# Performance work log

Hardware: AMD Instinct MI355X
Metric: run time of the kernel (lower is better)

## Reference

```python
import jax, jax.numpy as jnp
import numpy as np

# MX microscaling decode helpers. Codes are stored as int32 holding uint8 bit patterns.
_FP4_MAG = jnp.array([0.0, 0.5, 1.0, 1.5, 2.0, 3.0, 4.0, 6.0], dtype=jnp.float32)  # E2M1

def dec_fp4(c):
    # c in [0,16): bit3 = sign, bits0-2 index E2M1 magnitude LUT
    s = jnp.where(c >= 8, -1.0, 1.0)
    return s * _FP4_MAG[c & 7]

def dec_fp6(c):
    # E3M2, bias 3. bit5 sign, bits2-4 exp, bits0-1 mantissa
    s = jnp.where(c >= 32, -1.0, 1.0)
    e = ((c >> 2) & 7).astype(jnp.float32)
    m = (c & 3).astype(jnp.float32)
    mag = jnp.where(e == 0, m * 0.25 * 0.25, (1.0 + m * 0.25) * jnp.exp2(e - 3.0))
    return s * mag

def dec_fp8(c):
    # E4M3, bias 7. bit7 sign, bits3-6 exp, bits0-2 mantissa (NaN code decoded as 480, consistent both sides)
    s = jnp.where(c >= 128, -1.0, 1.0)
    e = ((c >> 3) & 15).astype(jnp.float32)
    m = (c & 7).astype(jnp.float32)
    mag = jnp.where(e == 0, m * 0.125 * jnp.exp2(-6.0), (1.0 + m * 0.125) * jnp.exp2(e - 7.0))
    return s * mag

def unpack4(p):
    # [..., K//2] bytes -> [..., K] nibbles; low nibble = even element, high = odd
    lo = p & 15
    hi = (p >> 4) & 15
    return jnp.stack([lo, hi], axis=-1).reshape(*p.shape[:-1], p.shape[-1] * 2)

def unpack6(p):
    # little-endian 6-bit packing: 4 values per 3 bytes. [..., K*6//8] -> [..., K]
    g = p.reshape(*p.shape[:-1], -1, 3)
    b0, b1, b2 = g[..., 0], g[..., 1], g[..., 2]
    v0 = b0 & 0x3F
    v1 = ((b0 >> 6) & 3) | ((b1 & 0x0F) << 2)
    v2 = ((b1 >> 4) & 0x0F) | ((b2 & 3) << 4)
    v3 = (b2 >> 2) & 0x3F
    return jnp.stack([v0, v1, v2, v3], axis=-1).reshape(*p.shape[:-1], p.shape[-1] * 4 // 3)

def blockscale(x, sf):
    # x [..., K] fp32, sf [..., K//32] E8M0 exponents: scale = 2^(sf-127) per 32-element block
    scale = jnp.exp2(sf.astype(jnp.float32) - 127.0)
    xs = x.reshape(*x.shape[:-1], -1, 32) * scale[..., None]
    return xs.reshape(x.shape)

def dequant(codes, sf, bits):
    if bits == 4:
        x = dec_fp4(unpack4(codes))
    elif bits == 6:
        x = dec_fp6(unpack6(codes))
    else:
        x = dec_fp8(codes)
    return blockscale(x, sf)


def setup_inputs() -> dict:
    key = jax.random.key(0)
    ks = jax.random.split(key, 13)
    M, N = 4096, 4096
    p4, p6, p8 = 3072, 768, 256
    ri = lambda k, sh: jax.random.randint(k, sh, 0, 256, dtype=jnp.int32)
    sf = lambda k, sh: jax.random.randint(k, sh, 121, 132, dtype=jnp.int32)
    return {
        "AN": ri(ks[0], (M, p4 // 2)),
        "AS": ri(ks[1], (M, p6 * 6 // 8)),
        "AO": ri(ks[2], (M, p8)),
        "SFAN": sf(ks[3], (M, p4 // 32)),
        "SFAS": sf(ks[4], (M, p6 // 32)),
        "SFAO": sf(ks[5], (M, p8 // 32)),
        "BN": ri(ks[6], (N, p4 // 2)),
        "BS": ri(ks[7], (N, p6 * 6 // 8)),
        "BO": ri(ks[8], (N, p8)),
        "SFBN": sf(ks[9], (N * p4 // 32,)),
        "SFBS": sf(ks[10], (N * p6 // 32,)),
        "SFBO": sf(ks[11], (N * p8 // 32,)),
        "bias": jax.random.normal(ks[12], (N,), dtype=jnp.float32) * 0.02,
    }


def reference(AN, AS, AO, SFAN, SFAS, SFAO, BN, BS, BO, SFBN, SFBS, SFBO, bias):
    N = BN.shape[0]
    a4 = dequant(AN, SFAN, 4)                       # [M, p4]
    w4 = dequant(BN, SFBN.reshape(N, -1), 4)        # [N, p4]
    a6 = dequant(AS, SFAS, 6)                       # [M, p6]
    w6 = dequant(BS, SFBS.reshape(N, -1), 6)        # [N, p6]
    a8 = dequant(AO, SFAO, 8)                       # [M, p8]
    w8 = dequant(BO, SFBO.reshape(N, -1), 8)        # [N, p8]
    y = a4 @ w4.T + a6 @ w6.T + a8 @ w8.T           # [M, N]
    return y + bias
```

## Files before the change

### kernel.cpp

```cpp
#include <hip/hip_runtime.h>

typedef short short8 __attribute__((ext_vector_type(8)));
typedef int   intx8  __attribute__((ext_vector_type(8)));
typedef float floatx16 __attribute__((ext_vector_type(16)));

__device__ __forceinline__ unsigned pk4(int a, int b, int c, int d) {
    return (a & 255) | ((b & 255) << 8) | ((c & 255) << 16) | ((unsigned)(d & 255) << 24);
}

__device__ __forceinline__ unsigned dec8bf(int c, int esf) {
    int s = (c & 128) << 8;
    int e = (c >> 3) & 15, m = c & 7;
    int rn = s | ((e + 120 + esf) << 7) | (m << 4);
    int nb = (m >= 4) ? 2 : ((m >= 2) ? 1 : 0);
    int rs = m ? (s | ((nb + 118 + esf) << 7) | ((m << (7 - nb)) & 0x7F)) : s;
    return (unsigned)(e ? rn : rs);
}

__device__ __forceinline__ void pack_one(
    int t, const int* __restrict__ Pn, const int* __restrict__ Ps, const int* __restrict__ Po,
    const int* __restrict__ Sn, const int* __restrict__ Ss, const int* __restrict__ So,
    unsigned char* __restrict__ C4, unsigned char* __restrict__ C6,
    unsigned short* __restrict__ C8, unsigned char* __restrict__ St, int R)
{
    int T0 = R * 48, T1 = T0 + R * 24, T2 = T1 + R * 8, T3 = T2 + R * 24, T4 = T3 + R * 12;
    if (t < T0) {
        int jj = t / R, r = t - jj * R;
        const int4* p = (const int4*)(Pn + (size_t)r * 1536 + jj * 32);
        #pragma unroll
        for (int h = 0; h < 2; ++h) {
            uint4 o; unsigned* po = (unsigned*)&o;
            #pragma unroll
            for (int q = 0; q < 4; q++) { int4 b = p[4 * h + q]; po[q] = pk4(b.x, b.y, b.z, b.w); }
            *(uint4*)(C4 + ((size_t)(2 * jj + h) * R + r) * 16) = o;
        }
    } else if (t < T1) {
        t -= T0; int g = t / R, r = t - g * R;
        const int4* p = (const int4*)(Ps + (size_t)r * 576 + g * 24);
        unsigned d[6];
        #pragma unroll
        for (int q = 0; q < 6; q++) { int4 b = p[q]; d[q] = pk4(b.x, b.y, b.z, b.w); }
        unsigned char* dst = C6 + ((size_t)g * R + r) * 24;
        *(int2*)(dst)      = (int2){ (int)d[0], (int)d[1] };
        *(int2*)(dst + 8)  = (int2){ (int)d[2], (int)d[3] };
        *(int2*)(dst + 16) = (int2){ (int)d[4], (int)d[5] };
    } else if (t < T2) {
        t -= T1; int jj = t / R, r = t - jj * R;
        const int4* p = (const int4*)(Po + (size_t)r * 256 + jj * 32);
        int e = So[r * 8 + jj] - 127;
        #pragma unroll
        for (int cq = 0; cq < 4; ++cq) {
            int4 c0 = p[2 * cq], c1 = p[2 * cq + 1];
            int cs[8] = { c0.x, c0.y, c0.z, c0.w, c1.x, c1.y, c1.z, c1.w };
            uint4 o; unsigned* po = (unsigned*)&o;
            #pragma unroll
            for (int i = 0; i < 4; i++)
                po[i] = dec8bf(cs[2 * i] & 255, e) | (dec8bf(cs[2 * i + 1] & 255, e) << 16);
            *(uint4*)((unsigned char*)C8 + ((size_t)(4 * jj + cq) * R + r) * 16) = o;
        }
    } else if (t < T3) {
        t -= T2; int q = t / R, r = t - q * R;
        int4 v = *(const int4*)(Sn + (size_t)r * 96 + q * 4);
        *(unsigned*)(St + ((size_t)q * R + r) * 4) = pk4(v.x, v.y, v.z, v.w);
    } else if (t < T4) {
        t -= T3; int b2 = t / R, r = t - b2 * R;
        int s0 = Ss[(size_t)r * 24 + 2 * b2] & 255, s1 = Ss[(size_t)r * 24 + 2 * b2 + 1] & 255;
        *(unsigned*)(St + ((size_t)(24 + b2) * R + r) * 4) = (unsigned)(s0 | (s1 << 8));
    }
}

__global__ __launch_bounds__(256) void pack_both(
    const int* __restrict__ AN, const int* __restrict__ AS, const int* __restrict__ AO,
    const int* __restrict__ SAn, const int* __restrict__ SAs, const int* __restrict__ SAo,
    unsigned char* __restrict__ A4, unsigned char* __restrict__ A6,
    unsigned short* __restrict__ A8, unsigned char* __restrict__ SaT, int M,
    const int* __restrict__ BN, const int* __restrict__ BS, const int* __restrict__ BO,
    const int* __restrict__ SBn, const int* __restrict__ SBs, const int* __restrict__ SBo,
    unsigned char* __restrict__ B4, unsigned char* __restrict__ B6,
    unsigned short* __restrict__ B8, unsigned char* __restrict__ SbT, int N)
{
    int t = blockIdx.x * 256 + threadIdx.x;
    int TA = M * 116;
    if (t < TA) pack_one(t, AN, AS, AO, SAn, SAs, SAo, A4, A6, A8, SaT, M);
    else        pack_one(t - TA, BN, BS, BO, SBn, SBs, SBo, B4, B6, B8, SbT, N);
}

__global__ __launch_bounds__(256, 2) void gemm_mx(
    const unsigned char* __restrict__ A4, const unsigned char* __restrict__ B4,
    const unsigned char* __restrict__ A6, const unsigned char* __restrict__ B6,
    const unsigned short* __restrict__ A8, const unsigned short* __restrict__ B8,
    const unsigned char* __restrict__ SaT, const unsigned char* __restrict__ SbT,
    const float* __restrict__ bias, float* __restrict__ C, int M, int N)
{
    int tid = threadIdx.x, w = tid >> 6, l = tid & 63;
    int bm = blockIdx.y, bn = blockIdx.x;
    int wm = (w >> 1) * 64, wn = (w & 1) * 64;
    int lr = l & 31, lh = l >> 5;

    floatx16 acc[2][2] = {};

    int rA[2] = { bm * 128 + wm + lr, bm * 128 + wm + 32 + lr };
    int cB[2] = { bn * 128 + wn + lr, bn * 128 + wn + 32 + lr };

    {
        unsigned strA = 32u * (unsigned)M, strB = 32u * (unsigned)N;
        unsigned fA0 = ((unsigned)lh * M + (unsigned)rA[0]) * 16u;
        unsigned fA1 = ((unsigned)lh * M + (unsigned)rA[1]) * 16u;
        unsigned fB0 = ((unsigned)lh * N + (unsigned)cB[0]) * 16u;
        unsigned fB1 = ((unsigned)lh * N + (unsigned)cB[1]) * 16u;

        int4 pa[4][2], pb[4][2];
        #pragma unroll
        for (int s = 0; s < 4; ++s) {
            pa[s][0] = *(const int4*)(A4 + fA0); pa[s][1] = *(const int4*)(A4 + fA1);
            pb[s][0] = *(const int4*)(B4 + fB0); pb[s][1] = *(const int4*)(B4 + fB1);
            fA0 += strA; fA1 += strA; fB0 += strB; fB1 += strB;
        }

        unsigned sstrA = 4u * (unsigned)M, sstrB = 4u * (unsigned)N;
        unsigned sA0 = (unsigned)rA[0] * 4u, sA1 = (unsigned)rA[1] * 4u;
        unsigned sB0 = (unsigned)cB[0] * 4u, sB1 = (unsigned)cB[1] * 4u;
        unsigned psa[2][2], psb[2][2];
        psa[0][0] = *(const unsigned*)(SaT + sA0);         psa[0][1] = *(const unsigned*)(SaT + sA1);
        psb[0][0] = *(const unsigned*)(SbT + sB0);         psb[0][1] = *(const unsigned*)(SbT + sB1);
        psa[1][0] = *(const unsigned*)(SaT + sA0 + sstrA); psa[1][1] = *(const unsigned*)(SaT + sA1 + sstrA);
        psb[1][0] = *(const unsigned*)(SbT + sB0 + sstrB); psb[1][1] = *(const unsigned*)(SbT + sB1 + sstrB);
        sA0 += 2 * sstrA; sA1 += 2 * sstrA; sB0 += 2 * sstrB; sB1 += 2 * sstrB;

        #pragma unroll 4
        for (int u = 0; u < 48; ++u) {
            int sl = u & 3, wsl = (u >> 1) & 1;
            int sh = 8 * ((u & 1) * 2 + lh);
            int sa0 = (int)((psa[wsl][0] >> sh) & 255), sa1 = (int)((psa[wsl][1] >> sh) & 255);
            int sb0 = (int)((psb[wsl][0] >> sh) & 255), sb1 = (int)((psb[wsl][1] >> sh) & 255);
            intx8 A0 = (intx8){ pa[sl][0].x, pa[sl][0].y, pa[sl][0].z, pa[sl][0].w, 0, 0, 0, 0 };
            intx8 A1 = (intx8){ pa[sl][1].x, pa[sl][1].y, pa[sl][1].z, pa[sl][1].w, 0, 0, 0, 0 };
            intx8 B0 = (intx8){ pb[sl][0].x, pb[sl][0].y, pb[sl][0].z, pb[sl][0].w, 0, 0, 0, 0 };
            intx8 B1 = (intx8){ pb[sl][1].x, pb[sl][1].y, pb[sl][1].z, pb[sl][1].w, 0, 0, 0, 0 };
            acc[0][0] = __builtin_amdgcn_mfma_scale_f32_32x32x64_f8f6f4(A0, B0, acc[0][0], 4, 4, 0, sa0, 0, sb0);
            acc[0][1] = __builtin_amdgcn_mfma_scale_f32_32x32x64_f8f6f4(A0, B1, acc[0][1], 4, 4, 0, sa0, 0, sb1);
            acc[1][0] = __builtin_amdgcn_mfma_scale_f32_32x32x64_f8f6f4(A1, B0, acc[1][0], 4, 4, 0, sa1, 0, sb0);
            acc[1][1] = __builtin_amdgcn_mfma_scale_f32_32x32x64_f8f6f4(A1, B1, acc[1][1], 4, 4, 0, sa1, 0, sb1);
            pa[sl][0] = *(const int4*)(A4 + fA0); pa[sl][1] = *(const int4*)(A4 + fA1);
            pb[sl][0] = *(const int4*)(B4 + fB0); pb[sl][1] = *(const int4*)(B4 + fB1);
            fA0 += strA; fA1 += strA; fB0 += strB; fB1 += strB;
            if (u & 1) {
                psa[wsl][0] = *(const unsigned*)(SaT + sA0); psa[wsl][1] = *(const unsigned*)(SaT + sA1);
                psb[wsl][0] = *(const unsigned*)(SbT + sB0); psb[wsl][1] = *(const unsigned*)(SbT + sB1);
                sA0 += sstrA; sA1 += sstrA; sB0 += sstrB; sB1 += sstrB;
            }
        }
    }

    {
        unsigned str6A = 48u * (unsigned)M, str6B = 48u * (unsigned)N;
        unsigned gA0 = ((unsigned)lh * M + (unsigned)rA[0]) * 24u;
        unsigned gA1 = ((unsigned)lh * M + (unsigned)rA[1]) * 24u;
        unsigned gB0 = ((unsigned)lh * N + (unsigned)cB[0]) * 24u;
        unsigned gB1 = ((unsigned)lh * N + (unsigned)cB[1]) * 24u;
        unsigned ss4A = 4u * (unsigned)M, ss4B = 4u * (unsigned)N;
        unsigned zA0 = (24u * (unsigned)M + (unsigned)rA[0]) * 4u;
        unsigned zA1 = (24u * (unsigned)M + (unsigned)rA[1]) * 4u;
        unsigned zB0 = (24u * (unsigned)N + (unsigned)cB[0]) * 4u;
        unsigned zB1 = (24u * (unsigned)N + (unsigned)cB[1]) * 4u;

        int2 qa[2][2][3], qb[2][2][3];
        unsigned p6a[2][2], p6b[2][2];
        #pragma unroll
        for (int s = 0; s < 2; ++s) {
            const unsigned char *a0 = A6 + gA0, *a1 = A6 + gA1, *b0 = B6 + gB0, *b1 = B6 + gB1;
            qa[s][0][0] = *(const int2*)(a0); qa[s][0][1] = *(const int2*)(a0 + 8); qa[s][0][2] = *(const int2*)(a0 + 16);
            qa[s][1][0] = *(const int2*)(a1); qa[s][1][1] = *(const int2*)(a1 + 8); qa[s][1][2] = *(const int2*)(a1 + 16);
            qb[s][0][0] = *(const int2*)(b0); qb[s][0][1] = *(const int2*)(b0 + 8); qb[s][0][2] = *(const int2*)(b0 + 16);
            qb[s][1][0] = *(const int2*)(b1); qb[s][1][1] = *(const int2*)(b1 + 8); qb[s][1][2] = *(const int2*)(b1 + 16);
            p6a[s][0] = *(const unsigned*)(SaT + zA0); p6a[s][1] = *(const unsigned*)(SaT + zA1);
            p6b[s][0] = *(const unsigned*)(SbT + zB0); p6b[s][1] = *(const unsigned*)(SbT + zB1);
            gA0 += str6A; gA1 += str6A; gB0 += str6B; gB1 += str6B;
            zA0 += ss4A; zA1 += ss4A; zB0 += ss4B; zB1 += ss4B;
        }
        int sh6 = 8 * lh;
        #pragma unroll 2
        for (int v = 0; v < 10; ++v) {
            int sl = v & 1;
            int sa0 = (int)((p6a[sl][0] >> sh6) & 255), sa1 = (int)((p6a[sl][1] >> sh6) & 255);
            int sb0 = (int)((p6b[sl][0] >> sh6) & 255), sb1 = (int)((p6b[sl][1] >> sh6) & 255);
            intx8 A0 = (intx8){ qa[sl][0][0].x, qa[sl][0][0].y, qa[sl][0][1].x, qa[sl][0][1].y, qa[sl][0][2].x, qa[sl][0][2].y, 0, 0 };
            intx8 A1 = (intx8){ qa[sl][1][0].x, qa[sl][1][0].y, qa[sl][1][1].x, qa[sl][1][1].y, qa[sl][1][2].x, qa[sl][1][2].y, 0, 0 };
            intx8 B0 = (intx8){ qb[sl][0][0].x, qb[sl][0][0].y, qb[sl][0][1].x, qb[sl][0][1].y, qb[sl][0][2].x, qb[sl][0][2].y, 0, 0 };
            intx8 B1 = (intx8){ qb[sl][1][0].x, qb[sl][1][0].y, qb[sl][1][1].x, qb[sl][1][1].y, qb[sl][1][2].x, qb[sl][1][2].y, 0, 0 };
            acc[0][0] = __builtin_amdgcn_mfma_scale_f32_32x32x64_f8f6f4(A0, B0, acc[0][0], 3, 3, 0, sa0, 0, sb0);
            acc[0][1] = __builtin_amdgcn_mfma_scale_f32_32x32x64_f8f6f4(A0, B1, acc[0][1], 3, 3, 0, sa0, 0, sb1);
            acc[1][0] = __builtin_amdgcn_mfma_scale_f32_32x32x64_f8f6f4(A1, B0, acc[1][0], 3, 3, 0, sa1, 0, sb0);
            acc[1][1] = __builtin_amdgcn_mfma_scale_f32_32x32x64_f8f6f4(A1, B1, acc[1][1], 3, 3, 0, sa1, 0, sb1);
            {
                const unsigned char *a0 = A6 + gA0, *a1 = A6 + gA1, *b0 = B6 + gB0, *b1 = B6 + gB1;
                qa[sl][0][0] = *(const int2*)(a0); qa[sl][0][1] = *(const int2*)(a0 + 8); qa[sl][0][2] = *(const int2*)(a0 + 16);
                qa[sl][1][0] = *(const int2*)(a1); qa[sl][1][1] = *(const int2*)(a1 + 8); qa[sl][1][2] = *(const int2*)(a1 + 16);
                qb[sl][0][0] = *(const int2*)(b0); qb[sl][0][1] = *(const int2*)(b0 + 8); qb[sl][0][2] = *(const int2*)(b0 + 16);
                qb[sl][1][0] = *(const int2*)(b1); qb[sl][1][1] = *(const int2*)(b1 + 8); qb[sl][1][2] = *(const int2*)(b1 + 16);
                p6a[sl][0] = *(const unsigned*)(SaT + zA0); p6a[sl][1] = *(const unsigned*)(SaT + zA1);
                p6b[sl][0] = *(const unsigned*)(SbT + zB0); p6b[sl][1] = *(const unsigned*)(SbT + zB1);
                gA0 += str6A; gA1 += str6A; gB0 += str6B; gB1 += str6B;
                zA0 += ss4A; zA1 += ss4A; zB0 += ss4B; zB1 += ss4B;
            }
        }
        #pragma unroll
        for (int v = 10; v < 12; ++v) {
            int sl = v & 1;
            int sa0 = (int)((p6a[sl][0] >> sh6) & 255), sa1 = (int)((p6a[sl][1] >> sh6) & 255);
            int sb0 = (int)((p6b[sl][0] >> sh6) & 255), sb1 = (int)((p6b[sl][1] >> sh6) & 255);
            intx8 A0 = (intx8){ qa[sl][0][0].x, qa[sl][0][0].y, qa[sl][0][1].x, qa[sl][0][1].y, qa[sl][0][2].x, qa[sl][0][2].y, 0, 0 };
            intx8 A1 = (intx8){ qa[sl][1][0].x, qa[sl][1][0].y, qa[sl][1][1].x, qa[sl][1][1].y, qa[sl][1][2].x, qa[sl][1][2].y, 0, 0 };
            intx8 B0 = (intx8){ qb[sl][0][0].x, qb[sl][0][0].y, qb[sl][0][1].x, qb[sl][0][1].y, qb[sl][0][2].x, qb[sl][0][2].y, 0, 0 };
            intx8 B1 = (intx8){ qb[sl][1][0].x, qb[sl][1][0].y, qb[sl][1][1].x, qb[sl][1][1].y, qb[sl][1][2].x, qb[sl][1][2].y, 0, 0 };
            acc[0][0] = __builtin_amdgcn_mfma_scale_f32_32x32x64_f8f6f4(A0, B0, acc[0][0], 3, 3, 0, sa0, 0, sb0);
            acc[0][1] = __builtin_amdgcn_mfma_scale_f32_32x32x64_f8f6f4(A0, B1, acc[0][1], 3, 3, 0, sa0, 0, sb1);
            acc[1][0] = __builtin_amdgcn_mfma_scale_f32_32x32x64_f8f6f4(A1, B0, acc[1][0], 3, 3, 0, sa1, 0, sb0);
            acc[1][1] = __builtin_amdgcn_mfma_scale_f32_32x32x64_f8f6f4(A1, B1, acc[1][1], 3, 3, 0, sa1, 0, sb1);
        }
    }

    {
        unsigned str8A = 32u * (unsigned)M, str8B = 32u * (unsigned)N;
        const unsigned char* A8b = (const unsigned char*)A8;
        const unsigned char* B8b = (const unsigned char*)B8;
        unsigned hA0 = ((unsigned)lh * M + (unsigned)rA[0]) * 16u;
        unsigned hA1 = ((unsigned)lh * M + (unsigned)rA[1]) * 16u;
        unsigned hB0 = ((unsigned)lh * N + (unsigned)cB[0]) * 16u;
        unsigned hB1 = ((unsigned)lh * N + (unsigned)cB[1]) * 16u;
        short8 ra[2][2], rb[2][2];
        #pragma unroll
        for (int s = 0; s < 2; ++s) {
            ra[s][0] = *(const short8*)(A8b + hA0); ra[s][1] = *(const short8*)(A8b + hA1);
            rb[s][0] = *(const short8*)(B8b + hB0); rb[s][1] = *(const short8*)(B8b + hB1);
            hA0 += str8A; hA1 += str8A; hB0 += str8B; hB1 += str8B;
        }
        #pragma unroll 2
        for (int q = 0; q < 16; ++q) {
            int sl = q & 1;
            acc[0][0] = __builtin_amdgcn_mfma_f32_32x32x16_bf16(ra[sl][0], rb[sl][0], acc[0][0], 0, 0, 0);
            acc[0][1] = __builtin_amdgcn_mfma_f32_32x32x16_bf16(ra[sl][0], rb[sl][1], acc[0][1], 0, 0, 0);
            acc[1][0] = __builtin_amdgcn_mfma_f32_32x32x16_bf16(ra[sl][1], rb[sl][0], acc[1][0], 0, 0, 0);
            acc[1][1] = __builtin_amdgcn_mfma_f32_32x32x16_bf16(ra[sl][1], rb[sl][1], acc[1][1], 0, 0, 0);
            ra[sl][0] = *(const short8*)(A8b + hA0); ra[sl][1] = *(const short8*)(A8b + hA1);
            rb[sl][0] = *(const short8*)(B8b + hB0); rb[sl][1] = *(const short8*)(B8b + hB1);
            hA0 += str8A; hA1 += str8A; hB0 += str8B; hB1 += str8B;
        }
    }

    #pragma unroll
    for (int i = 0; i < 2; i++)
        #pragma unroll
        for (int j = 0; j < 2; j++) {
            int col = bn * 128 + wn + j * 32 + lr;
            float bv = bias[col];
            #pragma unroll
            for (int r = 0; r < 16; r++) {
                int row = bm * 128 + wm + i * 32 + (r & 3) + 8 * (r >> 2) + 4 * lh;
                C[(size_t)row * N + col] = acc[i][j][r] + bv;
            }
        }
}

extern "C" void kernel_launch(void* const* d_in, const int* in_sizes, int n_in,
                              void* d_out, int out_size, void* d_ws, size_t ws_size,
                              hipStream_t stream) {
    const int* AN   = (const int*)d_in[0];
    const int* ASs  = (const int*)d_in[1];
    const int* AO   = (const int*)d_in[2];
    const int* SFAN = (const int*)d_in[3];
    const int* SFAS = (const int*)d_in[4];
    const int* SFAO = (const int*)d_in[5];
    const int* BN   = (const int*)d_in[6];
    const int* BS   = (const int*)d_in[7];
    const int* BO   = (const int*)d_in[8];
    const int* SFBN = (const int*)d_in[9];
    const int* SFBS = (const int*)d_in[10];
    const int* SFBO = (const int*)d_in[11];
    const float* bias = (const float*)d_in[12];

    int M = in_sizes[0] / 1536;
    int N = in_sizes[6] / 1536;

    unsigned char* ws = (unsigned char*)d_ws;
    size_t o = 0;
    unsigned char*  A4c = ws + o;                    o += (size_t)M * 1536;
    unsigned char*  B4c = ws + o;                    o += (size_t)N * 1536;
    unsigned char*  A6c = ws + o;                    o += (size_t)M * 576;
    unsigned char*  B6c = ws + o;                    o += (size_t)N * 576;
    unsigned short* A8d = (unsigned short*)(ws + o); o += (size_t)M * 512;
    unsigned short* B8d = (unsigned short*)(ws + o); o += (size_t)N * 512;
    unsigned char*  SaT = ws + o;                    o += (size_t)36 * M * 4;
    unsigned char*  SbT = ws + o;                    o += (size_t)36 * N * 4;

    int T = M * 116 + N * 116;
    pack_both<<<(T + 255) / 256, 256, 0, stream>>>(
        AN, ASs, AO, SFAN, SFAS, SFAO, A4c, A6c, A8d, SaT, M,
        BN, BS, BO, SFBN, SFBS, SFBO, B4c, B6c, B8d, SbT, N);

    dim3 grid(N / 128, M / 128);
    gemm_mx<<<grid, 256, 0, stream>>>(A4c, B4c, A6c, B6c, A8d, B8d,
                                      SaT, SbT, bias, (float*)d_out, M, N);
}
```

Measured before the change: 209.9 us.

## Coalesce pack reads, remap GEMM tiles per XCD, raise occupancy

The pack kernel now gives each thread one int4 of a source row, so neighbouring threads read contiguous input instead of striding across rows, at the cost of more threads and narrower 4/8-byte scattered writes. The GEMM remaps block indices so each XCD works on a compact 4x4-tile group, which is meant to improve L2 reuse of A and B panels. It also raises launch bounds to 3 blocks per CU and cuts the register prefetch ring from 4 to 3 stages, with unroll 12 to match the modulo-3 indexing. That trades prefetch depth for occupancy and risks register spills.

```diff
diff --git a/kernel.cpp b/kernel.cpp
--- a/kernel.cpp
+++ b/kernel.cpp
@@ -23,49 +23,32 @@
     unsigned char* __restrict__ C4, unsigned char* __restrict__ C6,
     unsigned short* __restrict__ C8, unsigned char* __restrict__ St, int R)
 {
-    int T0 = R * 48, T1 = T0 + R * 24, T2 = T1 + R * 8, T3 = T2 + R * 24, T4 = T3 + R * 12;
+    int T0 = R * 384, T1 = T0 + R * 144, T2 = T1 + R * 64, T3 = T2 + R * 24, T4 = T3 + R * 12;
     if (t < T0) {
-        int jj = t / R, r = t - jj * R;
-        const int4* p = (const int4*)(Pn + (size_t)r * 1536 + jj * 32);
-        #pragma unroll
-        for (int h = 0; h < 2; ++h) {
-            uint4 o; unsigned* po = (unsigned*)&o;
-            #pragma unroll
-            for (int q = 0; q < 4; q++) { int4 b = p[4 * h + q]; po[q] = pk4(b.x, b.y, b.z, b.w); }
-            *(uint4*)(C4 + ((size_t)(2 * jj + h) * R + r) * 16) = o;
-        }
+        int r = t / 384, i = t - r * 384;
+        int4 b = *(const int4*)(Pn + (size_t)r * 1536 + i * 4);
+        *(unsigned*)(C4 + ((size_t)(i >> 2) * R + r) * 16 + (i & 3) * 4) = pk4(b.x, b.y, b.z, b.w);
     } else if (t < T1) {
-        t -= T0; int g = t / R, r = t - g * R;
-        const int4* p = (const int4*)(Ps + (size_t)r * 576 + g * 24);
-        unsigned d[6];
-        #pragma unroll
-        for (int q = 0; q < 6; q++) { int4 b = p[q]; d[q] = pk4(b.x, b.y, b.z, b.w); }
-        unsigned char* dst = C6 + ((size_t)g * R + r) * 24;
-        *(int2*)(dst)      = (int2){ (int)d[0], (int)d[1] };
-        *(int2*)(dst + 8)  = (int2){ (int)d[2], (int)d[3] };
-        *(int2*)(dst + 16) = (int2){ (int)d[4], (int)d[5] };
+        t -= T0; int r = t / 144, i = t - r * 144;
+        int4 b = *(const int4*)(Ps + (size_t)r * 576 + i * 4);
+        *(unsigned*)(C6 + ((size_t)(i / 6) * R + r) * 24 + (i % 6) * 4) = pk4(b.x, b.y, b.z, b.w);
     } else if (t < T2) {
-        t -= T1; int jj = t / R, r = t - jj * R;
-        const int4* p = (const int4*)(Po + (size_t)r * 256 + jj * 32);
-        int e = So[r * 8 + jj] - 127;
-        #pragma unroll
-        for (int cq = 0; cq < 4; ++cq) {
-            int4 c0 = p[2 * cq], c1 = p[2 * cq + 1];
-            int cs[8] = { c0.x, c0.y, c0.z, c0.w, c1.x, c1.y, c1.z, c1.w };
-            uint4 o; unsigned* po = (unsigned*)&o;
-            #pragma unroll
-            for (int i = 0; i < 4; i++)
-                po[i] = dec8bf(cs[2 * i] & 255, e) | (dec8bf(cs[2 * i + 1] & 255, e) << 16);
-            *(uint4*)((unsigned char*)C8 + ((size_t)(4 * jj + cq) * R + r) * 16) = o;
-        }
+        t -= T1; int r = t / 64, i = t - r * 64;
+        int4 c = *(const int4*)(Po + (size_t)r * 256 + i * 4);
+        int e = So[r * 8 + (i >> 3)] - 127;
+        unsigned lo = dec8bf(c.x & 255, e) | (dec8bf(c.y & 255, e) << 16);
+        unsigned hi = dec8bf(c.z & 255, e) | (dec8bf(c.w & 255, e) << 16);
+        *(int2*)((unsigned char*)C8 + ((size_t)(i >> 1) * R + r) * 16 + (i & 1) * 8) =
+            (int2){ (int)lo, (int)hi };
     } else if (t < T3) {
-        t -= T2; int q = t / R, r = t - q * R;
+        t -= T2; int r = t / 24, q = t - r * 24;
         int4 v = *(const int4*)(Sn + (size_t)r * 96 + q * 4);
         *(unsigned*)(St + ((size_t)q * R + r) * 4) = pk4(v.x, v.y, v.z, v.w);
     } else if (t < T4) {
-        t -= T3; int b2 = t / R, r = t - b2 * R;
-        int s0 = Ss[(size_t)r * 24 + 2 * b2] & 255, s1 = Ss[(size_t)r * 24 + 2 * b2 + 1] & 255;
-        *(unsigned*)(St + ((size_t)(24 + b2) * R + r) * 4) = (unsigned)(s0 | (s1 << 8));
+        t -= T3; int r = t / 12, b2 = t - r * 12;
+        int2 sp = *(const int2*)(Ss + (size_t)r * 24 + 2 * b2);
+        *(unsigned*)(St + ((size_t)(24 + b2) * R + r) * 4) =
+            (unsigned)((sp.x & 255) | ((sp.y & 255) << 8));
     }
 }
 
@@ -80,12 +63,12 @@
     unsigned short* __restrict__ B8, unsigned char* __restrict__ SbT, int N)
 {
     int t = blockIdx.x * 256 + threadIdx.x;
-    int TA = M * 116;
+    int TA = M * 628;
     if (t < TA) pack_one(t, AN, AS, AO, SAn, SAs, SAo, A4, A6, A8, SaT, M);
     else        pack_one(t - TA, BN, BS, BO, SBn, SBs, SBo, B4, B6, B8, SbT, N);
 }
 
-__global__ __launch_bounds__(256, 2) void gemm_mx(
+__global__ __launch_bounds__(256, 3) void gemm_mx(
     const unsigned char* __restrict__ A4, const unsigned char* __restrict__ B4,
     const unsigned char* __restrict__ A6, const unsigned char* __restrict__ B6,
     const unsigned short* __restrict__ A8, const unsigned short* __restrict__ B8,
@@ -93,7 +76,16 @@
     const float* __restrict__ bias, float* __restrict__ C, int M, int N)
 {
     int tid = threadIdx.x, w = tid >> 6, l = tid & 63;
-    int bm = blockIdx.y, bn = blockIdx.x;
+    int nbm = M >> 7, nbn = N >> 7;
+    int bm, bn;
+    if (nbm == 32 && nbn == 32) {
+        int o = blockIdx.y * 32 + blockIdx.x;
+        int xcd = o & 7, pos = o >> 3;
+        int tile = pos >> 4, idx = pos & 15;
+        bm = xcd * 4 + (idx & 3);
+        bn = tile * 4 + (idx >> 2);
+    } else { bm = blockIdx.y; bn = blockIdx.x; }
+
     int wm = (w >> 1) * 64, wn = (w & 1) * 64;
     int lr = l & 31, lh = l >> 5;
 
@@ -109,9 +101,9 @@
         unsigned fB0 = ((unsigned)lh * N + (unsigned)cB[0]) * 16u;
         unsigned fB1 = ((unsigned)lh * N + (unsigned)cB[1]) * 16u;
 
-        int4 pa[4][2], pb[4][2];
-        #pragma unroll
-        for (int s = 0; s < 4; ++s) {
+        int4 pa[3][2], pb[3][2];
+        #pragma unroll
+        for (int s = 0; s < 3; ++s) {
             pa[s][0] = *(const int4*)(A4 + fA0); pa[s][1] = *(const int4*)(A4 + fA1);
             pb[s][0] = *(const int4*)(B4 + fB0); pb[s][1] = *(const int4*)(B4 + fB1);
             fA0 += strA; fA1 += strA; fB0 += strB; fB1 += strB;
@@ -127,9 +119,9 @@
         psb[1][0] = *(const unsigned*)(SbT + sB0 + sstrB); psb[1][1] = *(const unsigned*)(SbT + sB1 + sstrB);
         sA0 += 2 * sstrA; sA1 += 2 * sstrA; sB0 += 2 * sstrB; sB1 += 2 * sstrB;
 
-        #pragma unroll 4
+        #pragma unroll 12
         for (int u = 0; u < 48; ++u) {
-            int sl = u & 3, wsl = (u >> 1) & 1;
+            int sl = u % 3, wsl = (u >> 1) & 1;
             int sh = 8 * ((u & 1) * 2 + lh);
             int sa0 = (int)((psa[wsl][0] >> sh) & 255), sa1 = (int)((psa[wsl][1] >> sh) & 255);
             int sb0 = (int)((psb[wsl][0] >> sh) & 255), sb1 = (int)((psb[wsl][1] >> sh) & 255);
@@ -293,7 +285,7 @@
     unsigned char*  SaT = ws + o;                    o += (size_t)36 * M * 4;
     unsigned char*  SbT = ws + o;                    o += (size_t)36 * N * 4;
 
-    int T = M * 116 + N * 116;
+    int T = M * 628 + N * 628;
     pack_both<<<(T + 255) / 256, 256, 0, stream>>>(
         AN, ASs, AO, SFAN, SFAS, SFAO, A4c, A6c, A8d, SaT, M,
         BN, BS, BO, SFBN, SFBS, SFBO, B4c, B6c, B8d, SbT, N);
```

New measurement: 230.6 us. +9.9%, slower.
